# Kernel tuning notes

Hardware: AMD Instinct MI355X
Metric: run time of the kernel (lower is better)

## Reference

```python
import jax, jax.numpy as jnp
import numpy as np

D_MODEL = 2048
N_STATE = 256          # power of two
RANK = 64
LEVELS = int(np.log2(N_STATE))  # 8 butterfly levels
B, S = 4, 4096


def setup_inputs() -> dict:
    key = jax.random.key(0)
    ks = jax.random.split(key, 7)
    u = jax.random.normal(ks[0], (B, S, D_MODEL), dtype=jnp.float32)
    # stacked 2x2 butterfly factors, one per level (orthogonal-ish init)
    A_factors = jax.random.normal(ks[1], (LEVELS, 2, 2), dtype=jnp.float32)
    A_factors = A_factors / jnp.linalg.norm(A_factors, axis=-1, keepdims=True)
    W_b_rank = jax.random.normal(ks[2], (D_MODEL, RANK), dtype=jnp.float32) * (1.0 / np.sqrt(D_MODEL))
    W_b_state = jax.random.normal(ks[3], (RANK, N_STATE), dtype=jnp.float32) * (1.0 / np.sqrt(RANK))
    W_c_rank = jax.random.normal(ks[4], (N_STATE, RANK), dtype=jnp.float32) * (1.0 / np.sqrt(N_STATE))
    W_c_model = jax.random.normal(ks[5], (RANK, D_MODEL), dtype=jnp.float32) * (1.0 / np.sqrt(RANK))
    D_vec = jax.random.normal(ks[6], (D_MODEL,), dtype=jnp.float32) * 0.02
    return {"u": u, "A_factors": A_factors, "W_b_rank": W_b_rank,
            "W_b_state": W_b_state, "W_c_rank": W_c_rank,
            "W_c_model": W_c_model, "D_vec": D_vec}


def _apply_butterfly(state, A_factors):
    # state: [B, S, N]; reshape N into LEVELS axes of size 2 and apply a 2x2
    # factor along each axis (contracting the axis with A's FIRST dim, i.e.
    # x @ A, matching tf.matmul(flattened, factor)).
    b, s, n = state.shape
    x = state.reshape((b, s) + (2,) * LEVELS)
    for lvl in range(LEVELS):
        ax = 2 + lvl
        x = jnp.moveaxis(jnp.tensordot(x, A_factors[lvl], axes=[[ax], [0]]), -1, ax)
    return x.reshape(b, s, n)


def reference(u, A_factors, W_b_rank, W_b_state, W_c_rank, W_c_model, D_vec):
    # B path: low-rank projection to state space
    state = (u @ W_b_rank) @ W_b_state              # [B,S,N]
    # A: butterfly-structured state transform
    state = _apply_butterfly(state, A_factors)      # [B,S,N]
    # C path: low-rank projection back to model dim
    y = (state @ W_c_rank) @ W_c_model              # [B,S,D]
    # D: elementwise feedthrough
    return y + D_vec * u
```

## Files before the change

### kernel.cpp

```cpp
#include <hip/hip_runtime.h>

typedef unsigned short ushort_t;
typedef __attribute__((ext_vector_type(8))) short bf16x8;
typedef __attribute__((ext_vector_type(4))) float f32x4;
typedef __attribute__((ext_vector_type(4))) unsigned short us4;

#define DM 2048
#define RK 64

__device__ __forceinline__ ushort_t f2b(float f) {
    union { float f; unsigned u; } x; x.f = f;
    unsigned r = x.u + 0x7fff + ((x.u >> 16) & 1);
    return (ushort_t)(r >> 16);
}

__global__ void k_p1(const float* __restrict__ Wbs, const float* __restrict__ Af,
                     const float* __restrict__ Wcr, float* __restrict__ Mmid) {
    __shared__ float X[64 * 256];
    const int tid = threadIdx.x;
#pragma unroll
    for (int i = 0; i < 16; ++i) {
        int e = (i * 256 + tid) * 4;
        *(float4*)&X[e] = *(const float4*)&Wbs[e];
    }
    __syncthreads();
#pragma unroll
    for (int l = 0; l < 8; ++l) {
        const int bit = 1 << (7 - l);
        const float a00 = Af[l * 4 + 0], a01 = Af[l * 4 + 1];
        const float a10 = Af[l * 4 + 2], a11 = Af[l * 4 + 3];
#pragma unroll 4
        for (int p = 0; p < 32; ++p) {
            int pid = p * 256 + tid;
            int row = pid >> 7;
            int off = pid & 127;
            int lo = off & (bit - 1);
            int n0 = ((off ^ lo) << 1) | lo;
            int n1 = n0 | bit;
            float x0 = X[row * 256 + n0], x1 = X[row * 256 + n1];
            X[row * 256 + n0] = x0 * a00 + x1 * a10;
            X[row * 256 + n1] = x0 * a01 + x1 * a11;
        }
        __syncthreads();
    }
    int g = blockIdx.x * 256 + tid;
    int r1 = g >> 6, r2 = g & 63;
    float s = 0.f;
#pragma unroll 8
    for (int n = 0; n < 256; ++n) s += X[r1 * 256 + n] * Wcr[n * 64 + r2];
    Mmid[g] = s;
}

__global__ void k_p2(const float* __restrict__ Wbr, const float* __restrict__ Mmid,
                     const float* __restrict__ Wcm,
                     ushort_t* __restrict__ WeffT, ushort_t* __restrict__ WcT) {
    const int b = blockIdx.x, tid = threadIdx.x;
    if (b < 32) {
        __shared__ float LW[64][65];
        __shared__ float LM[64 * 64];
#pragma unroll
        for (int i = 0; i < 4; ++i) {
            int e = (i * 256 + tid) * 4;
            int kk = e >> 6, r = e & 63;
            float4 v = *(const float4*)&Wbr[(size_t)b * 4096 + e];
            LW[kk][r] = v.x; LW[kk][r + 1] = v.y; LW[kk][r + 2] = v.z; LW[kk][r + 3] = v.w;
        }
#pragma unroll
        for (int i = 0; i < 4; ++i) {
            int e = (i * 256 + tid) * 4;
            *(float4*)&LM[e] = *(const float4*)&Mmid[e];
        }
        __syncthreads();
        int kk = tid & 63, n0 = (tid >> 6) * 16;
        float acc[16];
#pragma unroll
        for (int j = 0; j < 16; ++j) acc[j] = 0.f;
        for (int r = 0; r < 64; ++r) {
            float wv = LW[kk][r];
            const float* mrow = &LM[r * 64 + n0];
            float4 m0 = *(const float4*)(mrow);
            float4 m1 = *(const float4*)(mrow + 4);
            float4 m2 = *(const float4*)(mrow + 8);
            float4 m3 = *(const float4*)(mrow + 12);
            acc[0] += wv * m0.x; acc[1] += wv * m0.y; acc[2] += wv * m0.z; acc[3] += wv * m0.w;
            acc[4] += wv * m1.x; acc[5] += wv * m1.y; acc[6] += wv * m1.z; acc[7] += wv * m1.w;
            acc[8] += wv * m2.x; acc[9] += wv * m2.y; acc[10] += wv * m2.z; acc[11] += wv * m2.w;
            acc[12] += wv * m3.x; acc[13] += wv * m3.y; acc[14] += wv * m3.z; acc[15] += wv * m3.w;
        }
#pragma unroll
        for (int j = 0; j < 16; ++j)
            WeffT[(size_t)(n0 + j) * DM + b * 64 + kk] = f2b(acc[j]);
    } else {
        __shared__ float LT[64][65];
        const int n0 = (b - 32) * 64;
#pragma unroll
        for (int i = 0; i < 4; ++i) {
            int e = (i * 256 + tid) * 4;
            int k = e >> 6, nn = e & 63;
            float4 v = *(const float4*)&Wcm[(size_t)k * DM + n0 + nn];
            LT[k][nn] = v.x; LT[k][nn + 1] = v.y; LT[k][nn + 2] = v.z; LT[k][nn + 3] = v.w;
        }
        __syncthreads();
#pragma unroll
        for (int i = 0; i < 4; ++i) {
            int e = (i * 256 + tid) * 4;
            int nn = e >> 6, k = e & 63;
            us4 o;
            o.x = f2b(LT[k][nn]); o.y = f2b(LT[k + 1][nn]);
            o.z = f2b(LT[k + 2][nn]); o.w = f2b(LT[k + 3][nn]);
            *(us4*)&WcT[(size_t)(n0 + nn) * RK + k] = o;
        }
    }
}

__global__ __launch_bounds__(256) void k_a(const float* __restrict__ u,
                                           const ushort_t* __restrict__ WeffT,
                                           ushort_t* __restrict__ tg) {
    __shared__ ushort_t Wl[64 * 256];

    const int tid = threadIdx.x;
    const int w = tid >> 6;
    const int lane = tid & 63;
    const int m16 = lane & 15;
    const int quad = lane >> 4;
    const size_t r0 = (size_t)blockIdx.x * 64;

    const float* ap = u + (r0 + w * 16 + m16) * DM + quad * 8;

    f32x4 acc[4];
#pragma unroll
    for (int j = 0; j < 4; ++j) acc[j] = (f32x4){0.f, 0.f, 0.f, 0.f};

    for (int s = 0; s < 8; ++s) {
        __syncthreads();
#pragma unroll
        for (int j = 0; j < 8; ++j) {
            int n = (w << 4) + j * 2 + (lane >> 5);
            int p = lane & 31;
            int chi = p ^ (n & 7);
            const ushort_t* gp = WeffT + (size_t)n * DM + s * 256 + chi * 8;
            __builtin_amdgcn_global_load_lds(
                (const __attribute__((address_space(1))) void*)gp,
                (__attribute__((address_space(3))) void*)&Wl[((w << 4) + j * 2) * 256],
                16, 0, 0);
        }
        __syncthreads();

#pragma unroll
        for (int c = 0; c < 8; ++c) {
            float4 u0 = *(const float4*)(ap + s * 256 + c * 32);
            float4 u1 = *(const float4*)(ap + s * 256 + c * 32 + 4);
            bf16x8 a;
            a[0] = (short)f2b(u0.x); a[1] = (short)f2b(u0.y);
            a[2] = (short)f2b(u0.z); a[3] = (short)f2b(u0.w);
            a[4] = (short)f2b(u1.x); a[5] = (short)f2b(u1.y);
            a[6] = (short)f2b(u1.z); a[7] = (short)f2b(u1.w);
#pragma unroll
            for (int j = 0; j < 4; ++j) {
                int n = m16 + 16 * j;
                int chi = ((c << 2) | quad) ^ (n & 7);
                bf16x8 b = *(const bf16x8*)&Wl[n * 256 + chi * 8];
                acc[j] = __builtin_amdgcn_mfma_f32_16x16x32_bf16(a, b, acc[j], 0, 0, 0);
            }
        }
    }

    __syncthreads();
    ushort_t* tt = Wl;
#pragma unroll
    for (int j = 0; j < 4; ++j)
#pragma unroll
        for (int i = 0; i < 4; ++i)
            tt[((w << 4) + quad * 4 + i) * 72 + 16 * j + m16] = f2b(acc[j][i]);
    __syncthreads();
    {
        const int lr = (w << 4) + m16;
        bf16x8 t0 = *(const bf16x8*)&tt[lr * 72 + quad * 16];
        bf16x8 t1 = *(const bf16x8*)&tt[lr * 72 + quad * 16 + 8];
        ushort_t* tp = tg + (r0 + lr) * RK + quad * 16;
        *(bf16x8*)tp = t0;
        *(bf16x8*)(tp + 8) = t1;
    }
}

__global__ __launch_bounds__(64) void k_b(const ushort_t* __restrict__ tg,
                                          const float* __restrict__ u,
                                          const ushort_t* __restrict__ WcT,
                                          const float* __restrict__ Dvec,
                                          float* __restrict__ out) {
    const int lane = threadIdx.x;
    const int m16 = lane & 15;
    const int quad = lane >> 4;
    const size_t r0 = (size_t)(blockIdx.x >> 4) * 256;
    const int c0 = (blockIdx.x & 15) * 128;

    bf16x8 wb0[8], wb1[8];
    float4 dvv[8];
#pragma unroll
    for (int ct = 0; ct < 8; ++ct) {
        const ushort_t* p = WcT + (size_t)(c0 + ct * 16 + m16) * RK + quad * 8;
        wb0[ct] = *(const bf16x8*)(p);
        wb1[ct] = *(const bf16x8*)(p + 32);
        dvv[ct] = *(const float4*)(Dvec + c0 + ct * 16 + quad * 4);
    }

    for (int g = 0; g < 16; ++g) {
        const size_t rg = r0 + g * 16;
        const ushort_t* tp = tg + (rg + m16) * RK + quad * 8;
        bf16x8 ta0 = *(const bf16x8*)(tp);
        bf16x8 ta1 = *(const bf16x8*)(tp + 32);
        const float* up = u + (rg + m16) * DM + c0 + quad * 4;
        float* op = out + (rg + m16) * DM + c0 + quad * 4;
#pragma unroll
        for (int ct = 0; ct < 8; ++ct) {
            f32x4 o = {0.f, 0.f, 0.f, 0.f};
            o = __builtin_amdgcn_mfma_f32_16x16x32_bf16(wb0[ct], ta0, o, 0, 0, 0);
            o = __builtin_amdgcn_mfma_f32_16x16x32_bf16(wb1[ct], ta1, o, 0, 0, 0);
            float4 uv = *(const float4*)(up + ct * 16);
            f32x4 st;
            st[0] = o[0] + dvv[ct].x * uv.x;
            st[1] = o[1] + dvv[ct].y * uv.y;
            st[2] = o[2] + dvv[ct].z * uv.z;
            st[3] = o[3] + dvv[ct].w * uv.w;
            *(f32x4*)(op + ct * 16) = st;
        }
    }
}

extern "C" void kernel_launch(void* const* d_in, const int* in_sizes, int n_in,
                              void* d_out, int out_size, void* d_ws, size_t ws_size,
                              hipStream_t stream) {
    (void)in_sizes; (void)n_in; (void)out_size; (void)ws_size;
    const float* u   = (const float*)d_in[0];
    const float* Af  = (const float*)d_in[1];
    const float* Wbr = (const float*)d_in[2];
    const float* Wbs = (const float*)d_in[3];
    const float* Wcr = (const float*)d_in[4];
    const float* Wcm = (const float*)d_in[5];
    const float* Dv  = (const float*)d_in[6];
    float* out = (float*)d_out;

    char* ws = (char*)d_ws;
    float*    Mmid  = (float*)(ws + 0);
    ushort_t* WeffT = (ushort_t*)(ws + 16384);
    ushort_t* WcT   = (ushort_t*)(ws + 278528);
    ushort_t* tg    = (ushort_t*)(ws + 540672);

    k_p1<<<16, 256, 0, stream>>>(Wbs, Af, Wcr, Mmid);
    k_p2<<<64, 256, 0, stream>>>(Wbr, Mmid, Wcm, WeffT, WcT);
    k_a <<<256, 256, 0, stream>>>(u, WeffT, tg);
    k_b <<<1024, 64, 0, stream>>>(tg, u, WcT, Dv, out);
}
```

Measured before the change: 342.1 us.

## Split k_a reduction across 8 waves with register-resident weights and LDS reduce

k_a now uses 512 threads. Each of its 8 waves owns a 256-wide K slice of the projection weights and holds that slice in registers instead of streaming it through LDS. Each wave processes 4 row groups of 16 and reduces partial sums across waves in shared memory. k_b is relaunched with twice as many blocks, each covering half as many rows, to raise parallelism. The aim is to remove the repeated LDS staging and its barriers on the weight, and to improve occupancy and latency hiding. The cost is heavy register use (32 bf16x8 weight fragments) and an extra cross-wave LDS reduction with two barriers per row group.

Result: faster. 319.5 us (-6.6%).

```diff
diff --git a/kernel.cpp b/kernel.cpp
--- a/kernel.cpp
+++ b/kernel.cpp
@@ -4,6 +4,7 @@
 typedef __attribute__((ext_vector_type(8))) short bf16x8;
 typedef __attribute__((ext_vector_type(4))) float f32x4;
 typedef __attribute__((ext_vector_type(4))) unsigned short us4;
+typedef __attribute__((ext_vector_type(2))) unsigned short us2;
 
 #define DM 2048
 #define RK 64
@@ -113,10 +114,10 @@
     }
 }
 
-__global__ __launch_bounds__(256) void k_a(const float* __restrict__ u,
+__global__ __launch_bounds__(512) void k_a(const float* __restrict__ u,
                                            const ushort_t* __restrict__ WeffT,
                                            ushort_t* __restrict__ tg) {
-    __shared__ ushort_t Wl[64 * 256];
+    __shared__ float red[8][64][20];
 
     const int tid = threadIdx.x;
     const int w = tid >> 6;
@@ -125,61 +126,54 @@
     const int quad = lane >> 4;
     const size_t r0 = (size_t)blockIdx.x * 64;
 
-    const float* ap = u + (r0 + w * 16 + m16) * DM + quad * 8;
-
-    f32x4 acc[4];
-#pragma unroll
-    for (int j = 0; j < 4; ++j) acc[j] = (f32x4){0.f, 0.f, 0.f, 0.f};
-
-    for (int s = 0; s < 8; ++s) {
-        __syncthreads();
-#pragma unroll
-        for (int j = 0; j < 8; ++j) {
-            int n = (w << 4) + j * 2 + (lane >> 5);
-            int p = lane & 31;
-            int chi = p ^ (n & 7);
-            const ushort_t* gp = WeffT + (size_t)n * DM + s * 256 + chi * 8;
-            __builtin_amdgcn_global_load_lds(
-                (const __attribute__((address_space(1))) void*)gp,
-                (__attribute__((address_space(3))) void*)&Wl[((w << 4) + j * 2) * 256],
-                16, 0, 0);
-        }
-        __syncthreads();
+    bf16x8 Wf[8][4];
+    {
+        const ushort_t* wbase = WeffT + (size_t)m16 * DM + w * 256 + quad * 8;
+#pragma unroll
+        for (int c = 0; c < 8; ++c)
+#pragma unroll
+            for (int j = 0; j < 4; ++j)
+                Wf[c][j] = *(const bf16x8*)(wbase + (size_t)j * 16 * DM + c * 32);
+    }
+
+    for (int g = 0; g < 4; ++g) {
+        const float* ap = u + (r0 + g * 16 + m16) * DM + w * 256 + quad * 8;
+        f32x4 acc[4];
+#pragma unroll
+        for (int j = 0; j < 4; ++j) acc[j] = (f32x4){0.f, 0.f, 0.f, 0.f};
 
 #pragma unroll
         for (int c = 0; c < 8; ++c) {
-            float4 u0 = *(const float4*)(ap + s * 256 + c * 32);
-            float4 u1 = *(const float4*)(ap + s * 256 + c * 32 + 4);
+            float4 u0 = *(const float4*)(ap + c * 32);
+            float4 u1 = *(const float4*)(ap + c * 32 + 4);
             bf16x8 a;
             a[0] = (short)f2b(u0.x); a[1] = (short)f2b(u0.y);
             a[2] = (short)f2b(u0.z); a[3] = (short)f2b(u0.w);
             a[4] = (short)f2b(u1.x); a[5] = (short)f2b(u1.y);
             a[6] = (short)f2b(u1.z); a[7] = (short)f2b(u1.w);
 #pragma unroll
-            for (int j = 0; j < 4; ++j) {
-                int n = m16 + 16 * j;
-                int chi = ((c << 2) | quad) ^ (n & 7);
-                bf16x8 b = *(const bf16x8*)&Wl[n * 256 + chi * 8];
-                acc[j] = __builtin_amdgcn_mfma_f32_16x16x32_bf16(a, b, acc[j], 0, 0, 0);
+            for (int j = 0; j < 4; ++j)
+                acc[j] = __builtin_amdgcn_mfma_f32_16x16x32_bf16(a, Wf[c][j], acc[j], 0, 0, 0);
+        }
+
+#pragma unroll
+        for (int j = 0; j < 4; ++j)
+            *(f32x4*)&red[w][16 * j + m16][quad * 4] = acc[j];
+        __syncthreads();
+
+        {
+            const int r = tid >> 5;
+            const int n0 = (tid & 31) * 2;
+            float s0 = 0.f, s1 = 0.f;
+#pragma unroll
+            for (int ww = 0; ww < 8; ++ww) {
+                s0 += red[ww][n0][r];
+                s1 += red[ww][n0 + 1][r];
             }
-        }
-    }
-
-    __syncthreads();
-    ushort_t* tt = Wl;
-#pragma unroll
-    for (int j = 0; j < 4; ++j)
-#pragma unroll
-        for (int i = 0; i < 4; ++i)
-            tt[((w << 4) + quad * 4 + i) * 72 + 16 * j + m16] = f2b(acc[j][i]);
-    __syncthreads();
-    {
-        const int lr = (w << 4) + m16;
-        bf16x8 t0 = *(const bf16x8*)&tt[lr * 72 + quad * 16];
-        bf16x8 t1 = *(const bf16x8*)&tt[lr * 72 + quad * 16 + 8];
-        ushort_t* tp = tg + (r0 + lr) * RK + quad * 16;
-        *(bf16x8*)tp = t0;
-        *(bf16x8*)(tp + 8) = t1;
+            us2 o; o.x = f2b(s0); o.y = f2b(s1);
+            *(us2*)&tg[(r0 + g * 16 + r) * RK + n0] = o;
+        }
+        __syncthreads();
     }
 }
 
@@ -191,7 +185,7 @@
     const int lane = threadIdx.x;
     const int m16 = lane & 15;
     const int quad = lane >> 4;
-    const size_t r0 = (size_t)(blockIdx.x >> 4) * 256;
+    const size_t r0 = (size_t)(blockIdx.x >> 4) * 128;
     const int c0 = (blockIdx.x & 15) * 128;
 
     bf16x8 wb0[8], wb1[8];
@@ -204,7 +198,7 @@
         dvv[ct] = *(const float4*)(Dvec + c0 + ct * 16 + quad * 4);
     }
 
-    for (int g = 0; g < 16; ++g) {
+    for (int g = 0; g < 8; ++g) {
         const size_t rg = r0 + g * 16;
         const ushort_t* tp = tg + (rg + m16) * RK + quad * 8;
         bf16x8 ta0 = *(const bf16x8*)(tp);
@@ -248,6 +242,6 @@
 
     k_p1<<<16, 256, 0, stream>>>(Wbs, Af, Wcr, Mmid);
     k_p2<<<64, 256, 0, stream>>>(Wbr, Mmid, Wcm, WeffT, WcT);
-    k_a <<<256, 256, 0, stream>>>(u, WeffT, tg);
-    k_b <<<1024, 64, 0, stream>>>(tg, u, WcT, Dv, out);
-}
+    k_a <<<256, 512, 0, stream>>>(u, WeffT, tg);
+    k_b <<<2048, 64, 0, stream>>>(tg, u, WcT, Dv, out);
+}
```
